# Performance work log

Measured on AMD Instinct MI355X. Metric: run time of the kernel, lower is better.

## Reference

```python
import jax, jax.numpy as jnp
import numpy as np

N_CAT = 10000   # n_categories
E = 128         # embedding_dim_c
D = 4           # n_demand
H = 128         # hidden_size
B = 32          # batch_size
S = 50          # max_session_len
I = 5000        # n_items (candidate pool)


def setup_inputs() -> dict:
    key = jax.random.key(0)
    ks = jax.random.split(key, 7)
    inp = jax.random.randint(ks[0], (B, S), 0, N_CAT)
    cand = jax.random.randint(ks[1], (I,), 0, N_CAT)
    emb_table = jax.random.normal(ks[2], (N_CAT, E), jnp.float32) * 0.02
    emb_table = emb_table.at[0].set(0.0)  # padding_idx=0
    W_demand = jax.random.normal(ks[3], (D * H, E), jnp.float32) / np.float32(np.sqrt(E))
    W_score = jax.random.normal(ks[4], (H, 2 * H), jnp.float32) / np.float32(np.sqrt(2 * H))  # torch [out,in]
    b_score = jax.random.normal(ks[5], (H,), jnp.float32) * 0.01
    w_score = jax.random.uniform(ks[6], (H,), jnp.float32, 0.0, 1.0 / np.float32(np.sqrt(H)))
    return {"input": inp, "candidate_pool_category": cand, "emb_table": emb_table,
            "W_demand": W_demand, "W_score": W_score, "b_score": b_score, "w_score": w_score}


def _forward(input, candidate_pool_category, emb_table, W_demand, W_score, b_score, w_score):
    h = w_score.shape[0]
    d = W_demand.shape[0] // h
    b, s = input.shape
    emb = emb_table[input]                                   # [B,S,E]
    hidden = (emb @ W_demand.T).reshape(b, s, d, h)          # [B,S,D,H] (hidden_key == hidden_demand)
    # demand_agg == 'exp': log(sum(exp(.), axis=seq))
    agg = jnp.log(jnp.sum(jnp.exp(hidden), axis=1))          # [B,D,H]
    # demand similarity loss: mean off-diagonal pairwise cosine similarity (batch-averaged)
    nrm = jnp.maximum(jnp.linalg.norm(agg, axis=-1, keepdims=True), 1e-8)
    u = agg / nrm
    gram = jnp.mean(jnp.einsum('bdh,beh->bde', u, u), axis=0)  # [D,D]
    off = 1.0 - jnp.eye(d, dtype=gram.dtype)
    demand_sim_loss = jnp.sum(gram * off) / (d * (d - 1))
    # split score Linear weight into demand/key halves (concat order: (agg, key))
    Wd, Wk = W_score[:, :h], W_score[:, h:]                  # each [H, H]
    agg_proj = agg @ Wd.T + b_score                          # [B,D,H]
    key_proj = jnp.einsum('bsdh,oh->bsdo', hidden, Wk)       # [B,S,D,H]
    demand_score = jnp.einsum('bsdh,h->bds',
                              jax.nn.relu(agg_proj[:, None] + key_proj), w_score)  # [B,D,S]
    cand_emb = emb_table[candidate_pool_category]            # [I,E]
    cand_hidden = (cand_emb @ W_demand.T).reshape(-1, d, h)  # [I,D,H]
    cand_proj = jnp.einsum('idh,oh->ido', cand_hidden, Wk)   # [I,D,H]
    demand_score_candidate = jnp.einsum('bdih,h->bdi',
                                        jax.nn.relu(agg_proj[:, :, None, :] + jnp.transpose(cand_proj, (1, 0, 2))[None]),
                                        w_score)             # [B,D,I]
    # score_act_fun is None -> no activation
    return demand_score, demand_score_candidate, emb, cand_emb, demand_sim_loss


def reference(input, candidate_pool_category, emb_table, W_demand, W_score, b_score, w_score):
    return _forward(input, candidate_pool_category, emb_table, W_demand, W_score, b_score, w_score)
```

## Files before the change

kernel.cpp:

```cpp
#include <hip/hip_runtime.h>

typedef __attribute__((ext_vector_type(8))) short short8;
typedef __attribute__((ext_vector_type(16))) float f32x16;

#define NROWS_IN 1600
#define NI 5000
#define BB 32
#define DDk 4
#define SS 50

__device__ __forceinline__ unsigned short f2bf(float f) {
    unsigned int u = __float_as_uint(f);
    u = (u + 0x7FFFu + ((u >> 16) & 1u)) >> 16;
    return (unsigned short)u;
}
__device__ __forceinline__ float b2f(unsigned short u) {
    return __uint_as_float(((unsigned int)u) << 16);
}

__global__ __launch_bounds__(256) void k_prep(const int* __restrict__ inp,
                                              const int* __restrict__ cand,
                                              const float* __restrict__ et,
                                              const float* __restrict__ Wd,
                                              const float* __restrict__ Ws,
                                              unsigned short* __restrict__ Wcat,
                                              unsigned short* __restrict__ Abf,
                                              float* __restrict__ o_emb,
                                              float* __restrict__ o_cemb) {
    int t = threadIdx.x;
    int blk = blockIdx.x;
    if (blk < 16) {
        const float4* src = (const float4*)Wd;
#pragma unroll
        for (int q = 0; q < 4; ++q) {
            int i = blk * 256 + t + q * 4096;
            float4 v = src[i];
            ushort4 o;
            o.x = f2bf(v.x); o.y = f2bf(v.y); o.z = f2bf(v.z); o.w = f2bf(v.w);
            *(ushort4*)(Wcat + (size_t)i * 4) = o;
        }
        return;
    }
    if (blk < 80) {
        __shared__ __align__(16) float sdw[128 * 128];
        __shared__ float wk[8][128];
        int cb = blk - 16;
        int d = cb >> 4, ot = cb & 15;
        const float4* src = (const float4*)(Wd + (size_t)d * 128 * 128);
#pragma unroll
        for (int q = 0; q < 16; ++q) {
            int i = t + q * 256;
            *(float4*)(&sdw[i * 4]) = src[i];
        }
        for (int x = t; x < 8 * 128; x += 256) {
            int ol = x >> 7, h = x & 127;
            wk[ol][h] = Ws[(ot * 8 + ol) * 256 + 128 + h];
        }
        __syncthreads();
        int e = t & 127, og = t >> 7;
        float acc[4] = {0.f, 0.f, 0.f, 0.f};
        for (int h = 0; h < 128; ++h) {
            float rd = sdw[h * 128 + e];
#pragma unroll
            for (int k = 0; k < 4; ++k) acc[k] += rd * wk[og * 4 + k][h];
        }
#pragma unroll
        for (int k = 0; k < 4; ++k) {
            int o = ot * 8 + og * 4 + k;
            Wcat[(size_t)(512 + d * 128 + o) * 128 + e] = f2bf(acc[k]);
        }
        return;
    }
    int pb = blk - 80;
    int r = pb * 8 + (t >> 5);
    int fc = t & 31;
    int id = (r < NROWS_IN) ? inp[r] : cand[r - NROWS_IN];
    float4 v = *(const float4*)(et + (size_t)id * 128 + fc * 4);
    if (r < NROWS_IN) *(float4*)(o_emb + (size_t)r * 128 + fc * 4) = v;
    else              *(float4*)(o_cemb + (size_t)(r - NROWS_IN) * 128 + fc * 4) = v;
    ushort4 o;
    o.x = f2bf(v.x); o.y = f2bf(v.y); o.z = f2bf(v.z); o.w = f2bf(v.w);
    *(ushort4*)(Abf + (size_t)r * 128 + fc * 4) = o;
}

__global__ __launch_bounds__(256) void k_fused_mid(const unsigned short* __restrict__ Abf,
                                                   const unsigned short* __restrict__ Wcat,
                                                   const float* __restrict__ Ws,
                                                   const float* __restrict__ bsc,
                                                   const float* __restrict__ wsc,
                                                   float* __restrict__ aggw,
                                                   float* __restrict__ apw,
                                                   float* __restrict__ o_ds) {
    __shared__ __align__(16) char lds[53536];
    unsigned short* sa   = (unsigned short*)lds;
    unsigned short* sb   = (unsigned short*)(lds + 16384);
    float*          skp  = (float*)lds;
    float*          sred = (float*)(lds + 49152);
    float*          sagg = (float*)(lds + 51712);
    float*          sap  = (float*)(lds + 52224);
    float*          spart= (float*)(lds + 52736);

    int b = blockIdx.x >> 2, d = blockIdx.x & 3;
    int t = threadIdx.x;
#pragma unroll
    for (int q = 0; q < 4; ++q) {
        int x = t + q * 256;
        int r = x >> 4, ch = x & 15;
        short8 v = {0, 0, 0, 0, 0, 0, 0, 0};
        if (r < SS) v = *(const short8*)(Abf + (size_t)(b * SS + r) * 128 + ch * 8);
        *(short8*)(sa + r * 128 + ((ch ^ (r & 15)) << 3)) = v;
    }
#pragma unroll
    for (int q = 0; q < 8; ++q) {
        int x = t + q * 256;
        int r = x >> 4, ch = x & 15;
        short8 v = *(const short8*)(Wcat + (size_t)(d * 128 + r) * 128 + ch * 8);
        *(short8*)(sb + r * 128 + ((ch ^ (r & 15)) << 3)) = v;
    }
    __syncthreads();

    int w = t >> 6, lane = t & 63;
    int lr = lane & 31, g = lane >> 5;
    int rt = w & 1, ct = w >> 1;
    int arow = rt * 32 + lr;
    int bcol0 = ct * 64 + lr, bcol1 = ct * 64 + 32 + lr;
    const unsigned short* pa  = sa + arow * 128;
    const unsigned short* pb0 = sb + bcol0 * 128;
    const unsigned short* pb1 = sb + bcol1 * 128;
    int axor = arow & 15, b0x = bcol0 & 15, b1x = bcol1 & 15;
    f32x16 h0 = {}, h1 = {};
#pragma unroll
    for (int ks = 0; ks < 8; ++ks) {
        int chA = ks * 2 + g;
        short8 a8 = *(const short8*)(pa  + ((chA ^ axor) << 3));
        short8 b8 = *(const short8*)(pb0 + ((chA ^ b0x) << 3));
        short8 c8 = *(const short8*)(pb1 + ((chA ^ b1x) << 3));
        h0 = __builtin_amdgcn_mfma_f32_32x32x16_bf16(a8, b8, h0, 0, 0, 0);
        h1 = __builtin_amdgcn_mfma_f32_32x32x16_bf16(a8, c8, h1, 0, 0, 0);
    }
    float p0 = 0.f, p1 = 0.f;
#pragma unroll
    for (int r = 0; r < 16; ++r) {
        int row = rt * 32 + (r & 3) + 8 * (r >> 2) + 4 * g;
        if (row < SS) { p0 += expf(h0[r]); p1 += expf(h1[r]); }
    }
    sred[bcol0 * 5 + rt * 2 + g] = p0;
    sred[bcol1 * 5 + rt * 2 + g] = p1;
    __syncthreads();
#pragma unroll
    for (int q = 0; q < 8; ++q) {
        int x = t + q * 256;
        int r = x >> 4, ch = x & 15;
        short8 v = *(const short8*)(Wcat + (size_t)(512 + d * 128 + r) * 128 + ch * 8);
        *(short8*)(sb + r * 128 + ((ch ^ (r & 15)) << 3)) = v;
    }
    if (t < 128) {
        float s = sred[t * 5] + sred[t * 5 + 1] + sred[t * 5 + 2] + sred[t * 5 + 3];
        float a = logf(s);
        sagg[t] = a;
        aggw[b * 512 + d * 128 + t] = a;
    }
    __syncthreads();
    f32x16 k0 = {}, k1 = {};
#pragma unroll
    for (int ks = 0; ks < 8; ++ks) {
        int chA = ks * 2 + g;
        short8 a8 = *(const short8*)(pa  + ((chA ^ axor) << 3));
        short8 b8 = *(const short8*)(pb0 + ((chA ^ b0x) << 3));
        short8 c8 = *(const short8*)(pb1 + ((chA ^ b1x) << 3));
        k0 = __builtin_amdgcn_mfma_f32_32x32x16_bf16(a8, b8, k0, 0, 0, 0);
        k1 = __builtin_amdgcn_mfma_f32_32x32x16_bf16(a8, c8, k1, 0, 0, 0);
    }
    if (t < 128) {
        const float* wr = Ws + t * 256;
        float acc = bsc[t];
        for (int ch = 0; ch < 32; ++ch) {
            float4 a4 = *(const float4*)(sagg + ch * 4);
            float4 w4 = *(const float4*)(wr + ch * 4);
            acc += a4.x * w4.x + a4.y * w4.y + a4.z * w4.z + a4.w * w4.w;
        }
        sap[t] = acc;
        apw[(b * DDk + d) * 128 + t] = acc;
    }
    __syncthreads();
#pragma unroll
    for (int r = 0; r < 16; ++r) {
        int row = rt * 32 + (r & 3) + 8 * (r >> 2) + 4 * g;
        int c0 = ct * 64 + lr, c1 = ct * 64 + 32 + lr;
        skp[row * 128 + ((((c0 >> 2) ^ (row & 7)) << 2) | (c0 & 3))] = k0[r];
        skp[row * 128 + ((((c1 >> 2) ^ (row & 7)) << 2) | (c1 & 3))] = k1[r];
    }
    __syncthreads();
    if (t < 200) {
        int s = t >> 2, oq = t & 3;
        float acc = 0.f;
#pragma unroll
        for (int c = 0; c < 8; ++c) {
            int ch = oq * 8 + c;
            float4 a4 = *(const float4*)(sap + ch * 4);
            float4 w4 = *(const float4*)(wsc + ch * 4);
            float4 k4 = *(const float4*)(&skp[s * 128 + ((ch ^ (s & 7)) << 2)]);
            acc += w4.x * fmaxf(a4.x + k4.x, 0.f) + w4.y * fmaxf(a4.y + k4.y, 0.f)
                 + w4.z * fmaxf(a4.z + k4.z, 0.f) + w4.w * fmaxf(a4.w + k4.w, 0.f);
        }
        spart[t] = acc;
    }
    __syncthreads();
    if (t < SS) {
        float v = spart[t * 4] + spart[t * 4 + 1] + spart[t * 4 + 2] + spart[t * 4 + 3];
        o_ds[b * (DDk * SS) + d * SS + t] = v;
    }
}

__global__ __launch_bounds__(256) void k_cand(const unsigned short* __restrict__ Abf,
                                              const unsigned short* __restrict__ Wcat,
                                              const float* __restrict__ apw,
                                              const float* __restrict__ aggw,
                                              const float* __restrict__ wsc,
                                              float* __restrict__ o_dsc,
                                              float* __restrict__ o_loss) {
    __shared__ __align__(16) char lds[66048];
    int gid = blockIdx.x;
    int t = threadIdx.x;
    if (gid >= 316) {
        float* nrm = (float*)lds;
        if (t < 128) {
            const float* a = aggw + t * 128;
            float s = 0.f;
            for (int h = 0; h < 128; ++h) s += a[h] * a[h];
            nrm[t] = fmaxf(sqrtf(s), 1e-8f);
        }
        __syncthreads();
        float lb = 0.f;
        if (t < 32) {
            const float* a = aggw + t * 512;
            float i0 = 1.f / nrm[t * 4 + 0], i1 = 1.f / nrm[t * 4 + 1];
            float i2 = 1.f / nrm[t * 4 + 2], i3 = 1.f / nrm[t * 4 + 3];
            for (int h = 0; h < 128; ++h) {
                float u0 = a[h] * i0, u1 = a[128 + h] * i1;
                float u2 = a[256 + h] * i2, u3 = a[384 + h] * i3;
                float v = u0 + u1 + u2 + u3;
                lb += v * v - (u0 * u0 + u1 * u1 + u2 * u2 + u3 * u3);
            }
        }
        for (int off = 32; off; off >>= 1) lb += __shfl_down(lb, off);
        if (t == 0) o_loss[0] = lb / (float)(BB * DDk * (DDk - 1));
        return;
    }
    unsigned short* sa    = (unsigned short*)lds;
    unsigned short* sw    = (unsigned short*)(lds + 16384);
    unsigned short* scp16 = (unsigned short*)lds;
    float*          sap   = (float*)(lds + 49152);
    float*          swv   = (float*)(lds + 65536);

    int tile = gid >> 2, d = gid & 3;
    int i0 = tile * 64;
#pragma unroll
    for (int q = 0; q < 4; ++q) {
        int x = t + q * 256;
        int r = x >> 4, ch = x & 15;
        short8 v = {0, 0, 0, 0, 0, 0, 0, 0};
        if (i0 + r < NI) v = *(const short8*)(Abf + (size_t)(NROWS_IN + i0 + r) * 128 + ch * 8);
        *(short8*)(sa + r * 128 + ((ch ^ (r & 15)) << 3)) = v;
    }
#pragma unroll
    for (int q = 0; q < 8; ++q) {
        int x = t + q * 256;
        int r = x >> 4, ch = x & 15;
        short8 v = *(const short8*)(Wcat + (size_t)(512 + d * 128 + r) * 128 + ch * 8);
        *(short8*)(sw + r * 128 + ((ch ^ (r & 15)) << 3)) = v;
    }
    if (t < 128) swv[t] = wsc[t];
#pragma unroll
    for (int q = 0; q < 4; ++q) {
        int x = t + q * 256;
        int b = x >> 5, ch = x & 31;
        float4 v = *(const float4*)(apw + (size_t)(b * 4 + d) * 128 + ch * 4);
        *(float4*)(&sap[b * 128 + ((ch ^ (b & 7)) << 2)]) = v;
    }
    __syncthreads();
    int w = t >> 6, lane = t & 63;
    int rbase = (w & 1) * 32, cbase = (w >> 1) * 64;
    int lr = lane & 31, g = lane >> 5;
    int arow = rbase + lr;
    int bcol0 = cbase + lr, bcol1 = cbase + 32 + lr;
    const unsigned short* pa  = sa + arow * 128;
    const unsigned short* pb0 = sw + bcol0 * 128;
    const unsigned short* pb1 = sw + bcol1 * 128;
    int axor = arow & 15, b0x = bcol0 & 15, b1x = bcol1 & 15;
    f32x16 acc0 = {}, acc1 = {};
#pragma unroll
    for (int ks = 0; ks < 8; ++ks) {
        int chA = ks * 2 + g;
        short8 a8 = *(const short8*)(pa  + ((chA ^ axor) << 3));
        short8 b8 = *(const short8*)(pb0 + ((chA ^ b0x) << 3));
        short8 c8 = *(const short8*)(pb1 + ((chA ^ b1x) << 3));
        acc0 = __builtin_amdgcn_mfma_f32_32x32x16_bf16(a8, b8, acc0, 0, 0, 0);
        acc1 = __builtin_amdgcn_mfma_f32_32x32x16_bf16(a8, c8, acc1, 0, 0, 0);
    }
    __syncthreads();
#pragma unroll
    for (int r = 0; r < 16; ++r) {
        int row = rbase + (r & 3) + 8 * (r >> 2) + 4 * g;
        int c0 = cbase + lr, c1 = cbase + 32 + lr;
        scp16[row * 128 + ((((c0 >> 2) ^ (row & 31)) << 2) | (c0 & 3))] = f2bf(acc0[r]);
        scp16[row * 128 + ((((c1 >> 2) ^ (row & 31)) << 2) | (c1 & 3))] = f2bf(acc1[r]);
    }
    __syncthreads();
    int b2 = t >> 4, gg = t & 15;
    float accA0 = 0.f, accA1 = 0.f, accA2 = 0.f, accA3 = 0.f;
    float accB0 = 0.f, accB1 = 0.f, accB2 = 0.f, accB3 = 0.f;
    const float* sapA = sap + b2 * 128;
    const float* sapB = sap + (b2 + 16) * 128;
    int bx = b2 & 7;
    for (int ch = 0; ch < 32; ++ch) {
        float4 w4 = *(const float4*)(swv + ch * 4);
        float4 aA = *(const float4*)(sapA + ((ch ^ bx) << 2));
        float4 aB = *(const float4*)(sapB + ((ch ^ bx) << 2));
#pragma unroll
        for (int kk = 0; kk < 4; ++kk) {
            int il = kk * 16 + gg;
            ushort4 cc = *(const ushort4*)(scp16 + il * 128 + ((ch ^ (il & 31)) << 2));
            float c0 = b2f(cc.x), c1 = b2f(cc.y), c2 = b2f(cc.z), c3 = b2f(cc.w);
            float pA = w4.x * fmaxf(aA.x + c0, 0.f) + w4.y * fmaxf(aA.y + c1, 0.f)
                     + w4.z * fmaxf(aA.z + c2, 0.f) + w4.w * fmaxf(aA.w + c3, 0.f);
            float pB = w4.x * fmaxf(aB.x + c0, 0.f) + w4.y * fmaxf(aB.y + c1, 0.f)
                     + w4.z * fmaxf(aB.z + c2, 0.f) + w4.w * fmaxf(aB.w + c3, 0.f);
            if (kk == 0) { accA0 += pA; accB0 += pB; }
            else if (kk == 1) { accA1 += pA; accB1 += pB; }
            else if (kk == 2) { accA2 += pA; accB2 += pB; }
            else { accA3 += pA; accB3 += pB; }
        }
    }
    {
        size_t baseA = (size_t)b2 * (DDk * NI) + d * NI;
        size_t baseB = (size_t)(b2 + 16) * (DDk * NI) + d * NI;
        int ia = i0 + gg;
        if (ia < NI)      { o_dsc[baseA + ia]      = accA0; o_dsc[baseB + ia]      = accB0; }
        if (ia + 16 < NI) { o_dsc[baseA + ia + 16] = accA1; o_dsc[baseB + ia + 16] = accB1; }
        if (ia + 32 < NI) { o_dsc[baseA + ia + 32] = accA2; o_dsc[baseB + ia + 32] = accB2; }
        if (ia + 48 < NI) { o_dsc[baseA + ia + 48] = accA3; o_dsc[baseB + ia + 48] = accB3; }
    }
}

extern "C" void kernel_launch(void* const* d_in, const int* in_sizes, int n_in,
                              void* d_out, int out_size, void* d_ws, size_t ws_size,
                              hipStream_t stream) {
    const int*   inp  = (const int*)d_in[0];
    const int*   cand = (const int*)d_in[1];
    const float* et   = (const float*)d_in[2];
    const float* Wd   = (const float*)d_in[3];
    const float* Ws   = (const float*)d_in[4];
    const float* bsc  = (const float*)d_in[5];
    const float* wsc  = (const float*)d_in[6];

    float* out = (float*)d_out;
    float* o_ds   = out;
    float* o_dsc  = out + 6400;
    float* o_emb  = out + 646400;
    float* o_cemb = out + 851200;
    float* o_loss = out + 1491200;

    char* wsb = (char*)d_ws;
    unsigned short* Wcat = (unsigned short*)wsb;
    unsigned short* Abf  = (unsigned short*)(wsb + 262144);
    float* aggw = (float*)(wsb + 2097152);
    float* apw  = aggw + 16384;

    hipLaunchKernelGGL(k_prep, dim3(905), dim3(256), 0, stream,
                       inp, cand, et, Wd, Ws, Wcat, Abf, o_emb, o_cemb);
    hipLaunchKernelGGL(k_fused_mid, dim3(128), dim3(256), 0, stream,
                       Abf, Wcat, Ws, bsc, wsc, aggw, apw, o_ds);
    hipLaunchKernelGGL(k_cand, dim3(317), dim3(256), 0, stream,
                       Abf, Wcat, apw, aggw, wsc, o_dsc, o_loss);
}
```

Baseline: 38.07 us.

## Fold prep kernel into consumers and split key projection into two GEMMs

Removes the separate prep kernel. Embedding gather, bf16 conversion and the emb/cand_emb output writes now happen inside the mid and candidate kernels, and W_demand and W_score are converted to bf16 on the fly. Instead of a precomputed W_demand·Wk product, each block runs two chained MFMA GEMMs: first the hidden projection, then rounding hidden to bf16 in LDS and multiplying by Wk. This saves a launch and the global round trip through workspace, at the cost of redundant weight conversion per block, an extra GEMM per block and an additional bf16 rounding of the intermediate hidden values.

New measurement: 39.14 us. 1.03x slower.

```diff
diff --git a/kernel.cpp b/kernel.cpp
--- a/kernel.cpp
+++ b/kernel.cpp
@@ -18,83 +18,21 @@
     return __uint_as_float(((unsigned int)u) << 16);
 }
 
-__global__ __launch_bounds__(256) void k_prep(const int* __restrict__ inp,
-                                              const int* __restrict__ cand,
+__global__ __launch_bounds__(256) void k_mid2(const int* __restrict__ inp,
                                               const float* __restrict__ et,
                                               const float* __restrict__ Wd,
                                               const float* __restrict__ Ws,
-                                              unsigned short* __restrict__ Wcat,
-                                              unsigned short* __restrict__ Abf,
+                                              const float* __restrict__ bsc,
+                                              const float* __restrict__ wsc,
                                               float* __restrict__ o_emb,
-                                              float* __restrict__ o_cemb) {
-    int t = threadIdx.x;
-    int blk = blockIdx.x;
-    if (blk < 16) {
-        const float4* src = (const float4*)Wd;
-#pragma unroll
-        for (int q = 0; q < 4; ++q) {
-            int i = blk * 256 + t + q * 4096;
-            float4 v = src[i];
-            ushort4 o;
-            o.x = f2bf(v.x); o.y = f2bf(v.y); o.z = f2bf(v.z); o.w = f2bf(v.w);
-            *(ushort4*)(Wcat + (size_t)i * 4) = o;
-        }
-        return;
-    }
-    if (blk < 80) {
-        __shared__ __align__(16) float sdw[128 * 128];
-        __shared__ float wk[8][128];
-        int cb = blk - 16;
-        int d = cb >> 4, ot = cb & 15;
-        const float4* src = (const float4*)(Wd + (size_t)d * 128 * 128);
-#pragma unroll
-        for (int q = 0; q < 16; ++q) {
-            int i = t + q * 256;
-            *(float4*)(&sdw[i * 4]) = src[i];
-        }
-        for (int x = t; x < 8 * 128; x += 256) {
-            int ol = x >> 7, h = x & 127;
-            wk[ol][h] = Ws[(ot * 8 + ol) * 256 + 128 + h];
-        }
-        __syncthreads();
-        int e = t & 127, og = t >> 7;
-        float acc[4] = {0.f, 0.f, 0.f, 0.f};
-        for (int h = 0; h < 128; ++h) {
-            float rd = sdw[h * 128 + e];
-#pragma unroll
-            for (int k = 0; k < 4; ++k) acc[k] += rd * wk[og * 4 + k][h];
-        }
-#pragma unroll
-        for (int k = 0; k < 4; ++k) {
-            int o = ot * 8 + og * 4 + k;
-            Wcat[(size_t)(512 + d * 128 + o) * 128 + e] = f2bf(acc[k]);
-        }
-        return;
-    }
-    int pb = blk - 80;
-    int r = pb * 8 + (t >> 5);
-    int fc = t & 31;
-    int id = (r < NROWS_IN) ? inp[r] : cand[r - NROWS_IN];
-    float4 v = *(const float4*)(et + (size_t)id * 128 + fc * 4);
-    if (r < NROWS_IN) *(float4*)(o_emb + (size_t)r * 128 + fc * 4) = v;
-    else              *(float4*)(o_cemb + (size_t)(r - NROWS_IN) * 128 + fc * 4) = v;
-    ushort4 o;
-    o.x = f2bf(v.x); o.y = f2bf(v.y); o.z = f2bf(v.z); o.w = f2bf(v.w);
-    *(ushort4*)(Abf + (size_t)r * 128 + fc * 4) = o;
-}
-
-__global__ __launch_bounds__(256) void k_fused_mid(const unsigned short* __restrict__ Abf,
-                                                   const unsigned short* __restrict__ Wcat,
-                                                   const float* __restrict__ Ws,
-                                                   const float* __restrict__ bsc,
-                                                   const float* __restrict__ wsc,
-                                                   float* __restrict__ aggw,
-                                                   float* __restrict__ apw,
-                                                   float* __restrict__ o_ds) {
+                                              float* __restrict__ aggw,
+                                              float* __restrict__ apw,
+                                              float* __restrict__ o_ds) {
     __shared__ __align__(16) char lds[53536];
     unsigned short* sa   = (unsigned short*)lds;
+    unsigned short* shid = (unsigned short*)lds;
     unsigned short* sb   = (unsigned short*)(lds + 16384);
-    float*          skp  = (float*)lds;
+    float*          skp  = (float*)(lds + 16384);
     float*          sred = (float*)(lds + 49152);
     float*          sagg = (float*)(lds + 51712);
     float*          sap  = (float*)(lds + 52224);
@@ -102,19 +40,40 @@
 
     int b = blockIdx.x >> 2, d = blockIdx.x & 3;
     int t = threadIdx.x;
+
 #pragma unroll
     for (int q = 0; q < 4; ++q) {
         int x = t + q * 256;
         int r = x >> 4, ch = x & 15;
         short8 v = {0, 0, 0, 0, 0, 0, 0, 0};
-        if (r < SS) v = *(const short8*)(Abf + (size_t)(b * SS + r) * 128 + ch * 8);
+        if (r < SS) {
+            int id = inp[b * SS + r];
+            const float* p = et + (size_t)id * 128 + ch * 8;
+            float4 v0 = *(const float4*)p;
+            float4 v1 = *(const float4*)(p + 4);
+            if (d == 0) {
+                float* eo = o_emb + (size_t)(b * SS + r) * 128 + ch * 8;
+                *(float4*)eo = v0; *(float4*)(eo + 4) = v1;
+            }
+            v[0] = (short)f2bf(v0.x); v[1] = (short)f2bf(v0.y);
+            v[2] = (short)f2bf(v0.z); v[3] = (short)f2bf(v0.w);
+            v[4] = (short)f2bf(v1.x); v[5] = (short)f2bf(v1.y);
+            v[6] = (short)f2bf(v1.z); v[7] = (short)f2bf(v1.w);
+        }
         *(short8*)(sa + r * 128 + ((ch ^ (r & 15)) << 3)) = v;
     }
 #pragma unroll
     for (int q = 0; q < 8; ++q) {
         int x = t + q * 256;
         int r = x >> 4, ch = x & 15;
-        short8 v = *(const short8*)(Wcat + (size_t)(d * 128 + r) * 128 + ch * 8);
+        const float* p = Wd + (size_t)(d * 128 + r) * 128 + ch * 8;
+        float4 v0 = *(const float4*)p;
+        float4 v1 = *(const float4*)(p + 4);
+        short8 v;
+        v[0] = (short)f2bf(v0.x); v[1] = (short)f2bf(v0.y);
+        v[2] = (short)f2bf(v0.z); v[3] = (short)f2bf(v0.w);
+        v[4] = (short)f2bf(v1.x); v[5] = (short)f2bf(v1.y);
+        v[6] = (short)f2bf(v1.z); v[7] = (short)f2bf(v1.w);
         *(short8*)(sb + r * 128 + ((ch ^ (r & 15)) << 3)) = v;
     }
     __syncthreads();
@@ -123,16 +82,16 @@
     int lr = lane & 31, g = lane >> 5;
     int rt = w & 1, ct = w >> 1;
     int arow = rt * 32 + lr;
+    int axor = arow & 15;
     int bcol0 = ct * 64 + lr, bcol1 = ct * 64 + 32 + lr;
-    const unsigned short* pa  = sa + arow * 128;
     const unsigned short* pb0 = sb + bcol0 * 128;
     const unsigned short* pb1 = sb + bcol1 * 128;
-    int axor = arow & 15, b0x = bcol0 & 15, b1x = bcol1 & 15;
+    int b0x = bcol0 & 15, b1x = bcol1 & 15;
     f32x16 h0 = {}, h1 = {};
 #pragma unroll
     for (int ks = 0; ks < 8; ++ks) {
         int chA = ks * 2 + g;
-        short8 a8 = *(const short8*)(pa  + ((chA ^ axor) << 3));
+        short8 a8 = *(const short8*)(sa + arow * 128 + ((chA ^ axor) << 3));
         short8 b8 = *(const short8*)(pb0 + ((chA ^ b0x) << 3));
         short8 c8 = *(const short8*)(pb1 + ((chA ^ b1x) << 3));
         h0 = __builtin_amdgcn_mfma_f32_32x32x16_bf16(a8, b8, h0, 0, 0, 0);
@@ -148,10 +107,24 @@
     sred[bcol1 * 5 + rt * 2 + g] = p1;
     __syncthreads();
 #pragma unroll
+    for (int r = 0; r < 16; ++r) {
+        int row = rt * 32 + (r & 3) + 8 * (r >> 2) + 4 * g;
+        int c0 = ct * 64 + lr, c1 = ct * 64 + 32 + lr;
+        shid[row * 128 + ((((c0 >> 3) ^ (row & 15)) << 3) | (c0 & 7))] = f2bf(h0[r]);
+        shid[row * 128 + ((((c1 >> 3) ^ (row & 15)) << 3) | (c1 & 7))] = f2bf(h1[r]);
+    }
+#pragma unroll
     for (int q = 0; q < 8; ++q) {
         int x = t + q * 256;
         int r = x >> 4, ch = x & 15;
-        short8 v = *(const short8*)(Wcat + (size_t)(512 + d * 128 + r) * 128 + ch * 8);
+        const float* p = Ws + (size_t)r * 256 + 128 + ch * 8;
+        float4 v0 = *(const float4*)p;
+        float4 v1 = *(const float4*)(p + 4);
+        short8 v;
+        v[0] = (short)f2bf(v0.x); v[1] = (short)f2bf(v0.y);
+        v[2] = (short)f2bf(v0.z); v[3] = (short)f2bf(v0.w);
+        v[4] = (short)f2bf(v1.x); v[5] = (short)f2bf(v1.y);
+        v[6] = (short)f2bf(v1.z); v[7] = (short)f2bf(v1.w);
         *(short8*)(sb + r * 128 + ((ch ^ (r & 15)) << 3)) = v;
     }
     if (t < 128) {
@@ -165,7 +138,7 @@
 #pragma unroll
     for (int ks = 0; ks < 8; ++ks) {
         int chA = ks * 2 + g;
-        short8 a8 = *(const short8*)(pa  + ((chA ^ axor) << 3));
+        short8 a8 = *(const short8*)(shid + arow * 128 + ((chA ^ axor) << 3));
         short8 b8 = *(const short8*)(pb0 + ((chA ^ b0x) << 3));
         short8 c8 = *(const short8*)(pb1 + ((chA ^ b1x) << 3));
         k0 = __builtin_amdgcn_mfma_f32_32x32x16_bf16(a8, b8, k0, 0, 0, 0);
@@ -212,13 +185,16 @@
     }
 }
 
-__global__ __launch_bounds__(256) void k_cand(const unsigned short* __restrict__ Abf,
-                                              const unsigned short* __restrict__ Wcat,
-                                              const float* __restrict__ apw,
-                                              const float* __restrict__ aggw,
-                                              const float* __restrict__ wsc,
-                                              float* __restrict__ o_dsc,
-                                              float* __restrict__ o_loss) {
+__global__ __launch_bounds__(256) void k_cand2(const int* __restrict__ cand,
+                                               const float* __restrict__ et,
+                                               const float* __restrict__ Wd,
+                                               const float* __restrict__ Ws,
+                                               const float* __restrict__ apw,
+                                               const float* __restrict__ aggw,
+                                               const float* __restrict__ wsc,
+                                               float* __restrict__ o_cemb,
+                                               float* __restrict__ o_dsc,
+                                               float* __restrict__ o_loss) {
     __shared__ __align__(16) char lds[66048];
     int gid = blockIdx.x;
     int t = threadIdx.x;
@@ -248,8 +224,9 @@
         return;
     }
     unsigned short* sa    = (unsigned short*)lds;
-    unsigned short* sw    = (unsigned short*)(lds + 16384);
-    unsigned short* scp16 = (unsigned short*)lds;
+    unsigned short* shid  = (unsigned short*)lds;
+    unsigned short* sb    = (unsigned short*)(lds + 16384);
+    unsigned short* scp16 = (unsigned short*)(lds + 16384);
     float*          sap   = (float*)(lds + 49152);
     float*          swv   = (float*)(lds + 65536);
 
@@ -260,15 +237,35 @@
         int x = t + q * 256;
         int r = x >> 4, ch = x & 15;
         short8 v = {0, 0, 0, 0, 0, 0, 0, 0};
-        if (i0 + r < NI) v = *(const short8*)(Abf + (size_t)(NROWS_IN + i0 + r) * 128 + ch * 8);
+        if (i0 + r < NI) {
+            int id = cand[i0 + r];
+            const float* p = et + (size_t)id * 128 + ch * 8;
+            float4 v0 = *(const float4*)p;
+            float4 v1 = *(const float4*)(p + 4);
+            if (d == 0) {
+                float* eo = o_cemb + (size_t)(i0 + r) * 128 + ch * 8;
+                *(float4*)eo = v0; *(float4*)(eo + 4) = v1;
+            }
+            v[0] = (short)f2bf(v0.x); v[1] = (short)f2bf(v0.y);
+            v[2] = (short)f2bf(v0.z); v[3] = (short)f2bf(v0.w);
+            v[4] = (short)f2bf(v1.x); v[5] = (short)f2bf(v1.y);
+            v[6] = (short)f2bf(v1.z); v[7] = (short)f2bf(v1.w);
+        }
         *(short8*)(sa + r * 128 + ((ch ^ (r & 15)) << 3)) = v;
     }
 #pragma unroll
     for (int q = 0; q < 8; ++q) {
         int x = t + q * 256;
         int r = x >> 4, ch = x & 15;
-        short8 v = *(const short8*)(Wcat + (size_t)(512 + d * 128 + r) * 128 + ch * 8);
-        *(short8*)(sw + r * 128 + ((ch ^ (r & 15)) << 3)) = v;
+        const float* p = Wd + (size_t)(d * 128 + r) * 128 + ch * 8;
+        float4 v0 = *(const float4*)p;
+        float4 v1 = *(const float4*)(p + 4);
+        short8 v;
+        v[0] = (short)f2bf(v0.x); v[1] = (short)f2bf(v0.y);
+        v[2] = (short)f2bf(v0.z); v[3] = (short)f2bf(v0.w);
+        v[4] = (short)f2bf(v1.x); v[5] = (short)f2bf(v1.y);
+        v[6] = (short)f2bf(v1.z); v[7] = (short)f2bf(v1.w);
+        *(short8*)(sb + r * 128 + ((ch ^ (r & 15)) << 3)) = v;
     }
     if (t < 128) swv[t] = wsc[t];
 #pragma unroll
@@ -279,20 +276,54 @@
         *(float4*)(&sap[b * 128 + ((ch ^ (b & 7)) << 2)]) = v;
     }
     __syncthreads();
+
     int w = t >> 6, lane = t & 63;
     int rbase = (w & 1) * 32, cbase = (w >> 1) * 64;
     int lr = lane & 31, g = lane >> 5;
     int arow = rbase + lr;
+    int axor = arow & 15;
     int bcol0 = cbase + lr, bcol1 = cbase + 32 + lr;
-    const unsigned short* pa  = sa + arow * 128;
-    const unsigned short* pb0 = sw + bcol0 * 128;
-    const unsigned short* pb1 = sw + bcol1 * 128;
-    int axor = arow & 15, b0x = bcol0 & 15, b1x = bcol1 & 15;
-    f32x16 acc0 = {}, acc1 = {};
+    const unsigned short* pb0 = sb + bcol0 * 128;
+    const unsigned short* pb1 = sb + bcol1 * 128;
+    int b0x = bcol0 & 15, b1x = bcol1 & 15;
+    f32x16 h0 = {}, h1 = {};
 #pragma unroll
     for (int ks = 0; ks < 8; ++ks) {
         int chA = ks * 2 + g;
-        short8 a8 = *(const short8*)(pa  + ((chA ^ axor) << 3));
+        short8 a8 = *(const short8*)(sa + arow * 128 + ((chA ^ axor) << 3));
+        short8 b8 = *(const short8*)(pb0 + ((chA ^ b0x) << 3));
+        short8 c8 = *(const short8*)(pb1 + ((chA ^ b1x) << 3));
+        h0 = __builtin_amdgcn_mfma_f32_32x32x16_bf16(a8, b8, h0, 0, 0, 0);
+        h1 = __builtin_amdgcn_mfma_f32_32x32x16_bf16(a8, c8, h1, 0, 0, 0);
+    }
+    __syncthreads();
+#pragma unroll
+    for (int r = 0; r < 16; ++r) {
+        int row = rbase + (r & 3) + 8 * (r >> 2) + 4 * g;
+        int c0 = cbase + lr, c1 = cbase + 32 + lr;
+        shid[row * 128 + ((((c0 >> 3) ^ (row & 15)) << 3) | (c0 & 7))] = f2bf(h0[r]);
+        shid[row * 128 + ((((c1 >> 3) ^ (row & 15)) << 3) | (c1 & 7))] = f2bf(h1[r]);
+    }
+#pragma unroll
+    for (int q = 0; q < 8; ++q) {
+        int x = t + q * 256;
+        int r = x >> 4, ch = x & 15;
+        const float* p = Ws + (size_t)r * 256 + 128 + ch * 8;
+        float4 v0 = *(const float4*)p;
+        float4 v1 = *(const float4*)(p + 4);
+        short8 v;
+        v[0] = (short)f2bf(v0.x); v[1] = (short)f2bf(v0.y);
+        v[2] = (short)f2bf(v0.z); v[3] = (short)f2bf(v0.w);
+        v[4] = (short)f2bf(v1.x); v[5] = (short)f2bf(v1.y);
+        v[6] = (short)f2bf(v1.z); v[7] = (short)f2bf(v1.w);
+        *(short8*)(sb + r * 128 + ((ch ^ (r & 15)) << 3)) = v;
+    }
+    __syncthreads();
+    f32x16 acc0 = {}, acc1 = {};
+#pragma unroll
+    for (int ks = 0; ks < 8; ++ks) {
+        int chA = ks * 2 + g;
+        short8 a8 = *(const short8*)(shid + arow * 128 + ((chA ^ axor) << 3));
         short8 b8 = *(const short8*)(pb0 + ((chA ^ b0x) << 3));
         short8 c8 = *(const short8*)(pb1 + ((chA ^ b1x) << 3));
         acc0 = __builtin_amdgcn_mfma_f32_32x32x16_bf16(a8, b8, acc0, 0, 0, 0);
@@ -326,10 +357,10 @@
                      + w4.z * fmaxf(aA.z + c2, 0.f) + w4.w * fmaxf(aA.w + c3, 0.f);
             float pB = w4.x * fmaxf(aB.x + c0, 0.f) + w4.y * fmaxf(aB.y + c1, 0.f)
                      + w4.z * fmaxf(aB.z + c2, 0.f) + w4.w * fmaxf(aB.w + c3, 0.f);
-            if (kk == 0) { accA0 += pA; accB0 += pB; }
+            if (kk == 0)      { accA0 += pA; accB0 += pB; }
             else if (kk == 1) { accA1 += pA; accB1 += pB; }
             else if (kk == 2) { accA2 += pA; accB2 += pB; }
-            else { accA3 += pA; accB3 += pB; }
+            else              { accA3 += pA; accB3 += pB; }
         }
     }
     {
@@ -361,16 +392,12 @@
     float* o_cemb = out + 851200;
     float* o_loss = out + 1491200;
 
-    char* wsb = (char*)d_ws;
-    unsigned short* Wcat = (unsigned short*)wsb;
-    unsigned short* Abf  = (unsigned short*)(wsb + 262144);
-    float* aggw = (float*)(wsb + 2097152);
-    float* apw  = aggw + 16384;
-
-    hipLaunchKernelGGL(k_prep, dim3(905), dim3(256), 0, stream,
-                       inp, cand, et, Wd, Ws, Wcat, Abf, o_emb, o_cemb);
-    hipLaunchKernelGGL(k_fused_mid, dim3(128), dim3(256), 0, stream,
-                       Abf, Wcat, Ws, bsc, wsc, aggw, apw, o_ds);
-    hipLaunchKernelGGL(k_cand, dim3(317), dim3(256), 0, stream,
-                       Abf, Wcat, apw, aggw, wsc, o_dsc, o_loss);
+    float* ws   = (float*)d_ws;
+    float* aggw = ws;
+    float* apw  = ws + 16384;
+
+    hipLaunchKernelGGL(k_mid2, dim3(128), dim3(256), 0, stream,
+                       inp, et, Wd, Ws, bsc, wsc, o_emb, aggw, apw, o_ds);
+    hipLaunchKernelGGL(k_cand2, dim3(317), dim3(256), 0, stream,
+                       cand, et, Wd, Ws, apw, aggw, wsc, o_cemb, o_dsc, o_loss);
 }
```
